# Performance work log

Measured on AMD Instinct MI355X. Metric: run time of the kernel, lower is better.

Reference implementation:

```python
import jax, jax.numpy as jnp
import numpy as np

N_HEADS = 16


def build_bd3lm_mask(n, block_size, dtype):
    """BD3LM mask for concatenated [xt | x0] input of length 2n.
    0 = attend, finfo.min = masked. Shape (2n, 2n)."""
    idx = jnp.arange(2 * n)
    q_idx = idx[:, None]
    kv_idx = idx[None, :]
    x0_q = q_idx >= n
    x0_kv = kv_idx >= n
    block_q = jnp.where(x0_q, (q_idx - n) // block_size, q_idx // block_size)
    block_kv = jnp.where(x0_kv, (kv_idx - n) // block_size, kv_idx // block_size)
    block_diagonal = (block_q == block_kv) & (x0_q == x0_kv)
    offset_block_causal = (block_q > block_kv) & x0_kv & (~x0_q)
    block_causal = (block_q >= block_kv) & x0_kv & x0_q
    can_attend = block_diagonal | offset_block_causal | block_causal
    neg = jnp.finfo(dtype).min
    return jnp.where(can_attend, jnp.array(0, dtype), jnp.array(neg, dtype))


def setup_inputs() -> dict:
    key = jax.random.key(0)
    ks = jax.random.split(key, 5)
    B, T, D = 4, 2048, 1024  # T = 2*L, L = 1024
    s = 1.0 / np.sqrt(D)
    return {
        "x": jax.random.normal(ks[0], (B, T, D), jnp.float32),
        "Wq": jax.random.normal(ks[1], (D, D), jnp.float32) * s,
        "bq": jnp.zeros((D,), jnp.float32),
        "Wk": jax.random.normal(ks[2], (D, D), jnp.float32) * s,
        "bk": jnp.zeros((D,), jnp.float32),
        "Wv": jax.random.normal(ks[3], (D, D), jnp.float32) * s,
        "bv": jnp.zeros((D,), jnp.float32),
        "Wo": jax.random.normal(ks[4], (D, D), jnp.float32) * s,
        "bo": jnp.zeros((D,), jnp.float32),
        "block_size": 4,
    }


def reference(x, Wq, bq, Wk, bk, Wv, bv, Wo, bo, block_size):
    B, T, D = x.shape
    H = N_HEADS
    hd = D // H
    n = T // 2  # length of each copy in [xt | x0]
    mask = build_bd3lm_mask(n, block_size, x.dtype)  # (T, T)

    def split_heads(t):  # (B, T, D) -> (B, H, T, hd)
        return t.reshape(B, T, H, hd).transpose(0, 2, 1, 3)

    q = split_heads(x @ Wq + bq) * (hd ** -0.5)
    k = split_heads(x @ Wk + bk)
    v = split_heads(x @ Wv + bv)
    scores = jnp.einsum("bhqd,bhkd->bhqk", q, k) + mask[None, None]
    attn = jax.nn.softmax(scores, axis=-1)
    ctx = jnp.einsum("bhqk,bhkd->bhqd", attn, v)
    ctx = ctx.transpose(0, 2, 1, 3).reshape(B, T, D)
    return ctx @ Wo + bo
```

## Files before the change

### kernel.cpp

```cpp
#include <hip/hip_runtime.h>
#include <hip/hip_bf16.h>
#include <stdint.h>

typedef __hip_bfloat16 bf16;
typedef short v8s __attribute__((ext_vector_type(8)));
typedef float v4f __attribute__((ext_vector_type(4)));

#define TT   2048
#define DD   1024
#define HH   16
#define HDIM 64
#define NN   1024
#define MASKV (-1e9f)
#define QSCALE 0.18033688011112042f

#if __has_builtin(__builtin_amdgcn_exp2f)
#define EXP2F(x) __builtin_amdgcn_exp2f(x)
#else
#define EXP2F(x) exp2f(x)
#endif

__device__ __forceinline__ v4f mfma16x16x32(v8s a, v8s b, v4f c) {
    return __builtin_amdgcn_mfma_f32_16x16x32_bf16(a, b, c, 0, 0, 0);
}

#define GLDS16(lds, g)                                                          \
    __builtin_amdgcn_global_load_lds(                                           \
        (const __attribute__((address_space(1))) void*)(g),                     \
        (__attribute__((address_space(3))) void*)(lds), 16, 0, 0)

__device__ __forceinline__ bf16 f2b(float f) { return __float2bfloat16(f); }

__global__ __launch_bounds__(256) void cast_x(const float* __restrict__ x,
                                              bf16* __restrict__ xb)
{
    const size_t i = ((size_t)blockIdx.x * 256 + threadIdx.x) * 4;
    const float4 f = *(const float4*)(x + i);
    union { bf16 b[4]; uint64_t u; } cv;
    cv.b[0] = f2b(f.x); cv.b[1] = f2b(f.y); cv.b[2] = f2b(f.z); cv.b[3] = f2b(f.w);
    *(uint64_t*)(xb + i) = cv.u;
}

__global__ __launch_bounds__(256) void transpose_w(
    const float* __restrict__ w0, const float* __restrict__ w1,
    const float* __restrict__ w2, const float* __restrict__ w3,
    bf16* __restrict__ dst)
{
    __shared__ float tile[64][65];
    const float* src = (blockIdx.z == 0) ? w0 : (blockIdx.z == 1) ? w1
                      : (blockIdx.z == 2) ? w2 : w3;
    bf16* d = dst + (size_t)blockIdx.z * 1024 * 1024;
    const int r0 = blockIdx.y * 64, c0 = blockIdx.x * 64;
    const int tx = threadIdx.x, ty = threadIdx.y;
#pragma unroll
    for (int j = 0; j < 16; j++) {
        int r = ty + j * 4;
        tile[r][tx] = src[(size_t)(r0 + r) * 1024 + c0 + tx];
    }
    __syncthreads();
#pragma unroll
    for (int j = 0; j < 16; j++) {
        int r = ty + j * 4;
        d[(size_t)(c0 + r) * 1024 + r0 + tx] = f2b(tile[tx][r]);
    }
}

__global__ __launch_bounds__(256) void transpose_v(
    const bf16* __restrict__ vtmp, bf16* __restrict__ vt)
{
    __shared__ bf16 tile[64][66];
    const int bh = blockIdx.y, t0 = blockIdx.x * 64;
    const int tx = threadIdx.x, ty = threadIdx.y;
    const bf16* src = vtmp + (size_t)bh * TT * HDIM;
    bf16* dst = vt + (size_t)bh * HDIM * TT;
#pragma unroll
    for (int j = 0; j < 16; j++) {
        int r = ty + j * 4;
        tile[r][tx] = src[(size_t)(t0 + r) * HDIM + tx];
    }
    __syncthreads();
#pragma unroll
    for (int j = 0; j < 16; j++) {
        int r = ty + j * 4;
        dst[(size_t)r * TT + t0 + tx] = tile[tx][r];
    }
}

__global__ __launch_bounds__(512, 2) void gemm_qkv(
    const bf16* __restrict__ A, const bf16* __restrict__ BT,
    const float* __restrict__ bq, const float* __restrict__ bk,
    const float* __restrict__ bv,
    bf16* __restrict__ qo, bf16* __restrict__ ko, bf16* __restrict__ vo)
{
    __shared__ __align__(16) bf16 As[2 * 256 * 64];
    __shared__ __align__(16) bf16 Bs[2 * 192 * 64];
    const int K = 1024, NT = K >> 6;

    const int id  = blockIdx.x;
    const int fid = (id & 7) * 64 + (id >> 3);
    const int by  = fid >> 4, bx = fid & 15;
    const int m0  = by * 256, n0 = bx * 192;

    const int tid  = threadIdx.x;
    const int lane = tid & 63, wv = tid >> 6;
    const int quad = lane >> 4, c = lane & 15;
    const int wm = wv >> 2, wn = wv & 3;
    const int c7 = c & 15 & 7;

    const int q8  = lane >> 3;
    const int gsw = ((lane & 7) ^ (q8 & 7)) << 3;
    const bf16* aSrc = A + (size_t)(m0 + wv * 8 + q8) * K + gsw;
    const int vB = wv * 8 + q8;
    const bf16* bSrc = BT + (size_t)(n0 + (vB >> 4) * 48 + (vB & 15)) * K + gsw;

    auto stageA = [&](bf16* dst, int j, int kt) {
        GLDS16(dst + (j * 64 + wv * 8) * 64, aSrc + (size_t)(j * 64) * K + kt * 64);
    };
    auto stageB = [&](bf16* dst, int j, int kt) {
        GLDS16(dst + (j * 64 + wv * 8) * 64, bSrc + (size_t)(j * 16) * K + kt * 64);
    };

    v4f acc[8][3];
#pragma unroll
    for (int i = 0; i < 8; i++)
#pragma unroll
        for (int j = 0; j < 3; j++) acc[i][j] = (v4f){0.f, 0.f, 0.f, 0.f};

    stageB(Bs, 0, 0); stageB(Bs, 1, 0);
    stageA(As, 0, 0); stageA(As, 2, 0);
    stageA(As, 1, 0); stageA(As, 3, 0);
    stageB(Bs, 2, 0);
    asm volatile("s_waitcnt vmcnt(3)" ::: "memory");
    asm volatile("s_barrier" ::: "memory");

    v8s afr[4][2], bfr01[2][2], bfr2[2];
#pragma unroll 1
    for (int kt = 0; kt < NT; ++kt) {
        bf16* Ac = As + (kt & 1) * 16384;
        bf16* Bc = Bs + (kt & 1) * 12288;
        bf16* An = As + ((kt & 1) ^ 1) * 16384;
        bf16* Bn = Bs + ((kt & 1) ^ 1) * 12288;
        const int ktn = (kt + 1 < NT) ? kt + 1 : kt;

#pragma unroll
        for (int nt = 0; nt < 2; nt++)
#pragma unroll
            for (int kh = 0; kh < 2; kh++)
                bfr01[nt][kh] = *(const v8s*)(Bc + (nt * 64 + wn * 16 + c) * 64
                                              + (((kh * 4 + quad) ^ c7) << 3));
#pragma unroll
        for (int mt = 0; mt < 4; mt++)
#pragma unroll
            for (int kh = 0; kh < 2; kh++)
                afr[mt][kh] = *(const v8s*)(Ac + (wm * 128 + mt * 16 + c) * 64
                                            + (((kh * 4 + quad) ^ c7) << 3));
        stageB(Bn, 0, ktn); stageB(Bn, 1, ktn);
        asm volatile("s_barrier" ::: "memory");
        __builtin_amdgcn_s_setprio(1);
#pragma unroll
        for (int mt = 0; mt < 4; mt++)
#pragma unroll
            for (int nt = 0; nt < 2; nt++) {
                acc[mt][nt] = mfma16x16x32(afr[mt][0], bfr01[nt][0], acc[mt][nt]);
                acc[mt][nt] = mfma16x16x32(afr[mt][1], bfr01[nt][1], acc[mt][nt]);
            }
        __builtin_amdgcn_s_setprio(0);
        asm volatile("s_waitcnt vmcnt(3)" ::: "memory");
        asm volatile("s_barrier" ::: "memory");

#pragma unroll
        for (int mt = 0; mt < 4; mt++)
#pragma unroll
            for (int kh = 0; kh < 2; kh++)
                afr[mt][kh] = *(const v8s*)(Ac + (wm * 128 + 64 + mt * 16 + c) * 64
                                            + (((kh * 4 + quad) ^ c7) << 3));
        stageA(An, 0, ktn); stageA(An, 2, ktn);
        asm volatile("s_barrier" ::: "memory");
        __builtin_amdgcn_s_setprio(1);
#pragma unroll
        for (int mt = 0; mt < 4; mt++)
#pragma unroll
            for (int nt = 0; nt < 2; nt++) {
                acc[4 + mt][nt] = mfma16x16x32(afr[mt][0], bfr01[nt][0], acc[4 + mt][nt]);
                acc[4 + mt][nt] = mfma16x16x32(afr[mt][1], bfr01[nt][1], acc[4 + mt][nt]);
            }
        __builtin_amdgcn_s_setprio(0);
        asm volatile("s_waitcnt vmcnt(4)" ::: "memory");
        asm volatile("s_barrier" ::: "memory");

#pragma unroll
        for (int kh = 0; kh < 2; kh++)
            bfr2[kh] = *(const v8s*)(Bc + (128 + wn * 16 + c) * 64
                                     + (((kh * 4 + quad) ^ c7) << 3));
        stageA(An, 1, ktn); stageA(An, 3, ktn);
        asm volatile("s_barrier" ::: "memory");
        __builtin_amdgcn_s_setprio(1);
#pragma unroll
        for (int mt = 0; mt < 4; mt++) {
            acc[4 + mt][2] = mfma16x16x32(afr[mt][0], bfr2[0], acc[4 + mt][2]);
            acc[4 + mt][2] = mfma16x16x32(afr[mt][1], bfr2[1], acc[4 + mt][2]);
        }
        __builtin_amdgcn_s_setprio(0);
        asm volatile("s_barrier" ::: "memory");

#pragma unroll
        for (int mt = 0; mt < 4; mt++)
#pragma unroll
            for (int kh = 0; kh < 2; kh++)
                afr[mt][kh] = *(const v8s*)(Ac + (wm * 128 + mt * 16 + c) * 64
                                            + (((kh * 4 + quad) ^ c7) << 3));
        stageB(Bn, 2, ktn);
        asm volatile("s_barrier" ::: "memory");
        __builtin_amdgcn_s_setprio(1);
#pragma unroll
        for (int mt = 0; mt < 4; mt++) {
            acc[mt][2] = mfma16x16x32(afr[mt][0], bfr2[0], acc[mt][2]);
            acc[mt][2] = mfma16x16x32(afr[mt][1], bfr2[1], acc[mt][2]);
        }
        __builtin_amdgcn_s_setprio(0);
        asm volatile("s_waitcnt vmcnt(3)" ::: "memory");
        asm volatile("s_barrier" ::: "memory");
    }
    asm volatile("s_waitcnt vmcnt(0)" ::: "memory");

#pragma unroll
    for (int i = 0; i < 8; i++)
#pragma unroll
        for (int nt = 0; nt < 3; nt++) {
            const int colb = n0 + wn * 48 + nt * 16;
            const int type = colb >> 10;
            bf16* o = (type == 0) ? qo : (type == 1) ? ko : vo;
            const float* bp = (type == 0) ? bq : (type == 1) ? bk : bv;
            const float scale = (type == 0) ? QSCALE : 1.0f;
            const int within = (colb & 1023) + c;
            const int h = within >> 6, d = within & 63;
            const float bias = bp[within];
#pragma unroll
            for (int r = 0; r < 4; r++) {
                const int row = m0 + wm * 128 + (i >> 2) * 64 + (i & 3) * 16
                                + quad * 4 + r;
                const int b_ = row >> 11, t = row & 2047;
                const int bh = b_ * HH + h;
                o[((size_t)bh * TT + t) * HDIM + d] =
                    f2b((acc[i][nt][r] + bias) * scale);
            }
        }
}

__device__ __forceinline__ void gemm_core_256x128(
    const bf16* __restrict__ A, const bf16* __restrict__ BT,
    const int m0, const int n0, const int K,
    bf16* __restrict__ As, bf16* __restrict__ Bs,
    v4f (&acc)[8][2])
{
    const int tid  = threadIdx.x;
    const int lane = tid & 63, wv = tid >> 6;
    const int quad = lane >> 4, c = lane & 15;
    const int wm = wv >> 2, wn = wv & 3;
    const int c7 = c & 7;
    const int NT = K >> 6;

    const int rloc = wv * 8 + (lane >> 3);
    const int gsw  = ((lane & 7) ^ ((lane >> 3) & 7)) << 3;
    const bf16* aSrc = A  + (size_t)(m0 + rloc) * K + gsw;
    const bf16* bSrc = BT + (size_t)(n0 + rloc) * K + gsw;

#pragma unroll
    for (int i = 0; i < 8; i++)
#pragma unroll
        for (int j = 0; j < 2; j++) acc[i][j] = (v4f){0.f, 0.f, 0.f, 0.f};

    auto stageA = [&](bf16* dst, int j, int kt) {
        const int mo = ((j & 1) << 7) | ((j >> 1) << 6);
        GLDS16(dst + (j * 64 + wv * 8) * 64, aSrc + (size_t)mo * K + kt * 64);
    };
    auto stageB = [&](bf16* dst, int j, int kt) {
        GLDS16(dst + (j * 64 + wv * 8) * 64, bSrc + (size_t)(j << 6) * K + kt * 64);
    };

    stageB(Bs, 0, 0); stageB(Bs, 1, 0);
    stageA(As, 0, 0); stageA(As, 1, 0); stageA(As, 2, 0); stageA(As, 3, 0);
    asm volatile("s_waitcnt vmcnt(2)" ::: "memory");
    asm volatile("s_barrier" ::: "memory");

#pragma unroll 1
    for (int kt = 0; kt < NT; ++kt) {
        bf16* Ac = As + (kt & 1) * 16384;
        bf16* Bc = Bs + (kt & 1) * 8192;
        bf16* An = As + ((kt & 1) ^ 1) * 16384;
        bf16* Bn = Bs + ((kt & 1) ^ 1) * 8192;
        const int ktn = (kt + 1 < NT) ? kt + 1 : kt;

        v8s bfr[2][2];
#pragma unroll
        for (int nt = 0; nt < 2; nt++)
#pragma unroll
            for (int kh = 0; kh < 2; kh++)
                bfr[nt][kh] = *(const v8s*)(Bc + (wn * 32 + nt * 16 + c) * 64
                                            + (((kh * 4 + quad) ^ c7) << 3));
        v8s af[4][2];
#pragma unroll
        for (int mt = 0; mt < 4; mt++)
#pragma unroll
            for (int kh = 0; kh < 2; kh++)
                af[mt][kh] = *(const v8s*)(Ac + (wm * 64 + mt * 16 + c) * 64
                                           + (((kh * 4 + quad) ^ c7) << 3));
        stageB(Bn, 0, ktn); stageB(Bn, 1, ktn); stageA(An, 0, ktn);
        asm volatile("s_barrier" ::: "memory");
        __builtin_amdgcn_s_setprio(1);
#pragma unroll
        for (int mt = 0; mt < 4; mt++)
#pragma unroll
            for (int nt = 0; nt < 2; nt++) {
                acc[mt][nt] = mfma16x16x32(af[mt][0], bfr[nt][0], acc[mt][nt]);
                acc[mt][nt] = mfma16x16x32(af[mt][1], bfr[nt][1], acc[mt][nt]);
            }
        __builtin_amdgcn_s_setprio(0);
        asm volatile("s_waitcnt vmcnt(3)" ::: "memory");
        asm volatile("s_barrier" ::: "memory");

#pragma unroll
        for (int mt = 0; mt < 4; mt++)
#pragma unroll
            for (int kh = 0; kh < 2; kh++)
                af[mt][kh] = *(const v8s*)(Ac + (128 + wm * 64 + mt * 16 + c) * 64
                                           + (((kh * 4 + quad) ^ c7) << 3));
        stageA(An, 1, ktn); stageA(An, 2, ktn); stageA(An, 3, ktn);
        asm volatile("s_barrier" ::: "memory");
        __builtin_amdgcn_s_setprio(1);
#pragma unroll
        for (int mt = 0; mt < 4; mt++)
#pragma unroll
            for (int nt = 0; nt < 2; nt++) {
                acc[4 + mt][nt] = mfma16x16x32(af[mt][0], bfr[nt][0], acc[4 + mt][nt]);
                acc[4 + mt][nt] = mfma16x16x32(af[mt][1], bfr[nt][1], acc[4 + mt][nt]);
            }
        __builtin_amdgcn_s_setprio(0);
        asm volatile("s_waitcnt vmcnt(2)" ::: "memory");
        asm volatile("s_barrier" ::: "memory");
    }
}

__global__ __launch_bounds__(512, 2) void gemm_out(
    const bf16* __restrict__ A, const bf16* __restrict__ BT,
    const float* __restrict__ bo, float* __restrict__ out)
{
    __shared__ __align__(16) bf16 As[2 * 256 * 64];
    __shared__ __align__(16) bf16 Bs[2 * 128 * 64];
    const int id  = blockIdx.x;
    const int fid = (id & 7) * 32 + (id >> 3);
    const int by  = fid >> 3, bx = fid & 7;
    const int m0  = by * 256, n0 = bx * 128;

    v4f acc[8][2];
    gemm_core_256x128(A, BT, m0, n0, 1024, As, Bs, acc);

    const int tid  = threadIdx.x;
    const int lane = tid & 63, wv = tid >> 6;
    const int quad = lane >> 4, c = lane & 15;
    const int wm = wv >> 2, wn = wv & 3;

#pragma unroll
    for (int mt = 0; mt < 8; mt++)
#pragma unroll
        for (int nt = 0; nt < 2; nt++) {
            const int col = n0 + wn * 32 + nt * 16 + c;
            const float bias = bo[col];
#pragma unroll
            for (int r = 0; r < 4; r++) {
                const int row = m0 + wm * 128 + mt * 16 + quad * 4 + r;
                out[(size_t)row * 1024 + col] = acc[mt][nt][r] + bias;
            }
        }
}

__global__ __launch_bounds__(256, 4) void attn(
    const bf16* __restrict__ Q, const bf16* __restrict__ Kb,
    const bf16* __restrict__ VT, bf16* __restrict__ ctx,
    const int* __restrict__ bsp)
{
    __shared__ __align__(16) bf16 Kt[2][32 * 64];
    __shared__ __align__(16) bf16 Vt[2][64 * 32];
    __shared__ __align__(16) bf16 plds[4][2][16 * 32];

    const int bs = bsp[0];
    const float inv  = 1.0f / (float)bs;
    const float hinv = 0.5f * inv;
    const int tid = threadIdx.x, lane = tid & 63, wv = tid >> 6;
    const int quad = lane >> 4, c = lane & 15;
    const int bh = blockIdx.x & 63;
    const int j  = blockIdx.x >> 6;
    const int g_tbl[16] = {7,6,5,4, 0,1,2,3, 4,5,6,7, 3,2,1,0};
    const bool xt = j < 8;
    const int g  = g_tbl[j];
    const int q0g = (xt ? 0 : NN) + g * 128;

    const bf16* qp = Q  + (size_t)bh * TT * HDIM;
    const bf16* kp = Kb + (size_t)bh * TT * HDIM;
    const bf16* vp = VT + (size_t)bh * HDIM * TT;

    int d_lo = 0, nd = 0, nf = 0, b_lo = 0, nb = 0;
    if (xt) {
        d_lo = (bs * (q0g / bs)) & ~31;
        const int d_hi = min((bs * ((q0g + 127) / bs) + bs + 31) & ~31, NN);
        nd = (d_hi - d_lo) >> 5;
        const int f = bs * (q0g / bs);
        nf = f >> 5;
        b_lo = NN + (nf << 5);
        const int b_hi = NN + min((bs * ((q0g + 127) / bs) + 31) & ~31, NN);
        nb = (b_hi > b_lo) ? (b_hi - b_lo) >> 5 : 0;
    } else {
        const int q0l = q0g - NN;
        const int f = min(bs * (q0l / bs) + bs, NN);
        nf = f >> 5;
        b_lo = NN + (nf << 5);
        const int b_hi = NN + min((bs * ((q0l + 127) / bs) + bs + 31) & ~31, NN);
        nb = (b_hi > b_lo) ? (b_hi - b_lo) >> 5 : 0;
    }
    const int nc = nd + nf + nb;

    float bqv[2][4];
#pragma unroll
    for (int t = 0; t < 2; t++)
#pragma unroll
        for (int r = 0; r < 4; r++) {
            const int qrow = q0g + wv * 32 + t * 16 + quad * 4 + r;
            const int qloc = xt ? qrow : qrow - NN;
            bqv[t][r] = floorf(fmaf((float)qloc, inv, hinv));
        }

    v8s aq[2][2];
#pragma unroll
    for (int t = 0; t < 2; t++) {
        const int rowb = q0g + wv * 32 + t * 16;
        aq[t][0] = *(const v8s*)(qp + (size_t)(rowb + c) * HDIM + quad * 8);
        aq[t][1] = *(const v8s*)(qp + (size_t)(rowb + c) * HDIM + 32 + quad * 8);
    }

    v4f O[2][4];
#pragma unroll
    for (int t = 0; t < 2; t++)
#pragma unroll
        for (int dt = 0; dt < 4; dt++) O[t][dt] = (v4f){0.f, 0.f, 0.f, 0.f};
    float lr[2][4] = {{0.f,0.f,0.f,0.f},{0.f,0.f,0.f,0.f}};

    const int klrow = lane >> 3, ks8 = lane & 7;
    const bf16* kSrc0 = kp + (size_t)(wv * 8 + klrow) * HDIM + ((ks8 ^ klrow) << 3);
    const int vlrow = lane >> 2, vs8 = lane & 3;
    const bf16* vSrc0 = vp + (size_t)(wv * 16 + vlrow) * TT + ((vs8 ^ (vlrow & 3)) << 3);

    auto kb_of = [&](int i, int& kb, int& type) {
        if (i < nd)           { kb = d_lo + (i << 5);             type = 1; }
        else if (i < nd + nf) { kb = NN + ((i - nd) << 5);        type = 0; }
        else                  { kb = b_lo + ((i - nd - nf) << 5); type = xt ? 2 : 3; }
    };
    auto stage = [&](int i) {
        int kb, ty; kb_of(i, kb, ty);
        const int sel = i & 1;
        GLDS16(&Kt[sel][wv * 512], kSrc0 + (size_t)kb * HDIM);
        GLDS16(&Vt[sel][wv * 512], vSrc0 + kb);
    };

    stage(0);
    asm volatile("s_waitcnt vmcnt(0)" ::: "memory");
    asm volatile("s_barrier" ::: "memory");

    const int xk = c & 7, xv = c & 3;
    const int pquad = quad << 3;
#pragma unroll 1
    for (int i = 0; i < nc; i++) {
        int kb, type; kb_of(i, kb, type);
        const int sel = i & 1;
        const bf16* Kl = Kt[sel];
        const bf16* Vl = Vt[sel];

        const v8s k0a = *(const v8s*)(Kl + c * 64        + ((quad       ^ xk) << 3));
        const v8s k0b = *(const v8s*)(Kl + c * 64        + (((quad ^ 4) ^ xk) << 3));
        const v8s k1a = *(const v8s*)(Kl + (16 + c) * 64 + ((quad       ^ xk) << 3));
        const v8s k1b = *(const v8s*)(Kl + (16 + c) * 64 + (((quad ^ 4) ^ xk) << 3));
        v8s vf[4];
#pragma unroll
        for (int dt = 0; dt < 4; dt++)
            vf[dt] = *(const v8s*)(Vl + (dt * 16 + c) * 32 + ((quad ^ xv) << 3));

        if (i + 1 < nc) stage(i + 1);

        float bkA = 0.f, bkB = 0.f;
        if (type) {
            const int off = (type == 1) ? 0 : NN;
            bkA = floorf(fmaf((float)(kb + c - off),      inv, hinv));
            bkB = floorf(fmaf((float)(kb + 16 + c - off), inv, hinv));
        }

#pragma unroll
        for (int t = 0; t < 2; t++) {
            v4f Sa = (v4f){0.f, 0.f, 0.f, 0.f};
            v4f Sb = (v4f){0.f, 0.f, 0.f, 0.f};
            Sa = mfma16x16x32(aq[t][0], k0a, Sa);
            Sa = mfma16x16x32(aq[t][1], k0b, Sa);
            Sb = mfma16x16x32(aq[t][0], k1a, Sb);
            Sb = mfma16x16x32(aq[t][1], k1b, Sb);
            bf16* pw = &plds[wv][t][(quad * 4) * 32];
#pragma unroll
            for (int r = 0; r < 4; r++) {
                float sa = Sa[r], sb = Sb[r];
                if (type == 1) {
                    if (bkA != bqv[t][r]) sa = MASKV;
                    if (bkB != bqv[t][r]) sb = MASKV;
                } else if (type == 2) {
                    if (!(bkA < bqv[t][r])) sa = MASKV;
                    if (!(bkB < bqv[t][r])) sb = MASKV;
                } else if (type == 3) {
                    if (!(bkA <= bqv[t][r])) sa = MASKV;
                    if (!(bkB <= bqv[t][r])) sb = MASKV;
                }
                const float pa = EXP2F(sa);
                const float pb = EXP2F(sb);
                lr[t][r] += pa + pb;
                pw[r * 32 + (c ^ pquad)]        = f2b(pa);
                pw[r * 32 + ((c + 16) ^ pquad)] = f2b(pb);
            }
        }
        asm volatile("s_waitcnt lgkmcnt(0)" ::: "memory");
#pragma unroll
        for (int t = 0; t < 2; t++) {
            const v8s pf = *(const v8s*)(&plds[wv][t][c * 32 +
                                        ((quad ^ ((c >> 2) & 3)) << 3)]);
#pragma unroll
            for (int dt = 0; dt < 4; dt++)
                O[t][dt] = mfma16x16x32(pf, vf[dt], O[t][dt]);
        }

        asm volatile("s_waitcnt vmcnt(0)" ::: "memory");
        asm volatile("s_barrier" ::: "memory");
    }

    const int b_ = bh >> 4, h = bh & 15;
#pragma unroll
    for (int t = 0; t < 2; t++)
#pragma unroll
        for (int r = 0; r < 4; r++) {
            float s = lr[t][r];
#pragma unroll
            for (int off = 1; off < 16; off <<= 1) s += __shfl_xor(s, off);
            const float invl = 1.0f / fmaxf(s, 1e-30f);
            const int trow = q0g + wv * 32 + t * 16 + quad * 4 + r;
#pragma unroll
            for (int dt = 0; dt < 4; dt++)
                ctx[((size_t)(b_ * TT + trow)) * DD + h * 64 + dt * 16 + c] =
                    f2b(O[t][dt][r] * invl);
        }
}

extern "C" void kernel_launch(void* const* d_in, const int* in_sizes, int n_in,
                              void* d_out, int out_size, void* d_ws, size_t ws_size,
                              hipStream_t stream)
{
    const float* x  = (const float*)d_in[0];
    const float* Wq = (const float*)d_in[1];
    const float* bq = (const float*)d_in[2];
    const float* Wk = (const float*)d_in[3];
    const float* bk = (const float*)d_in[4];
    const float* Wv = (const float*)d_in[5];
    const float* bv = (const float*)d_in[6];
    const float* Wo = (const float*)d_in[7];
    const float* bo = (const float*)d_in[8];
    const int*  bsp = (const int*)d_in[9];
    float* out = (float*)d_out;

    bf16* ws    = (bf16*)d_ws;
    bf16* xb    = ws;
    bf16* wqkvT = xb + 8388608;
    bf16* woT   = wqkvT + 3 * 1024 * 1024;
    bf16* qbuf  = woT + 1024 * 1024;
    bf16* kbuf  = qbuf + 8388608;
    bf16* vtmp  = kbuf + 8388608;
    bf16* vt    = vtmp + 8388608;
    bf16* ctx   = xb;

    cast_x<<<8192, 256, 0, stream>>>(x, xb);
    transpose_w<<<dim3(16, 16, 4), dim3(64, 4), 0, stream>>>(Wq, Wk, Wv, Wo, wqkvT);
    gemm_qkv<<<512, 512, 0, stream>>>(xb, wqkvT, bq, bk, bv, qbuf, kbuf, vtmp);
    transpose_v<<<dim3(32, 64), dim3(64, 4), 0, stream>>>(vtmp, vt);
    attn<<<1024, 256, 0, stream>>>(qbuf, kbuf, vt, ctx, bsp);
    gemm_out<<<256, 512, 0, stream>>>(ctx, woT, bo, out);
}
```

Baseline: 239.4 us.

## Fuse V transpose into QKV GEMM epilogue and triple-buffer attention K/V

The QKV GEMM epilogue now writes V directly in transposed (bh, d, t) layout with packed 8-byte stores of four consecutive tokens. This removes the separate transpose_v kernel and its extra read and write of V. The attention kernel moves from double to triple buffering of K/V tiles in LDS, prefetching two chunks ahead and waiting with vmcnt(2) instead of vmcnt(0), so load latency overlaps more compute. The costs are more LDS per block, which could lower occupancy, and redundant restaging of the last chunk near the tail.

```diff
diff --git a/kernel.cpp b/kernel.cpp
--- a/kernel.cpp
+++ b/kernel.cpp
@@ -65,32 +65,11 @@
     }
 }
 
-__global__ __launch_bounds__(256) void transpose_v(
-    const bf16* __restrict__ vtmp, bf16* __restrict__ vt)
-{
-    __shared__ bf16 tile[64][66];
-    const int bh = blockIdx.y, t0 = blockIdx.x * 64;
-    const int tx = threadIdx.x, ty = threadIdx.y;
-    const bf16* src = vtmp + (size_t)bh * TT * HDIM;
-    bf16* dst = vt + (size_t)bh * HDIM * TT;
-#pragma unroll
-    for (int j = 0; j < 16; j++) {
-        int r = ty + j * 4;
-        tile[r][tx] = src[(size_t)(t0 + r) * HDIM + tx];
-    }
-    __syncthreads();
-#pragma unroll
-    for (int j = 0; j < 16; j++) {
-        int r = ty + j * 4;
-        dst[(size_t)r * TT + t0 + tx] = tile[tx][r];
-    }
-}
-
 __global__ __launch_bounds__(512, 2) void gemm_qkv(
     const bf16* __restrict__ A, const bf16* __restrict__ BT,
     const float* __restrict__ bq, const float* __restrict__ bk,
     const float* __restrict__ bv,
-    bf16* __restrict__ qo, bf16* __restrict__ ko, bf16* __restrict__ vo)
+    bf16* __restrict__ qo, bf16* __restrict__ ko, bf16* __restrict__ vt)
 {
     __shared__ __align__(16) bf16 As[2 * 256 * 64];
     __shared__ __align__(16) bf16 Bs[2 * 192 * 64];
@@ -105,7 +84,7 @@
     const int lane = tid & 63, wv = tid >> 6;
     const int quad = lane >> 4, c = lane & 15;
     const int wm = wv >> 2, wn = wv & 3;
-    const int c7 = c & 15 & 7;
+    const int c7 = c & 7;
 
     const int q8  = lane >> 3;
     const int gsw = ((lane & 7) ^ (q8 & 7)) << 3;
@@ -221,7 +200,6 @@
         asm volatile("s_waitcnt vmcnt(3)" ::: "memory");
         asm volatile("s_barrier" ::: "memory");
     }
-    asm volatile("s_waitcnt vmcnt(0)" ::: "memory");
 
 #pragma unroll
     for (int i = 0; i < 8; i++)
@@ -229,20 +207,27 @@
         for (int nt = 0; nt < 3; nt++) {
             const int colb = n0 + wn * 48 + nt * 16;
             const int type = colb >> 10;
-            bf16* o = (type == 0) ? qo : (type == 1) ? ko : vo;
-            const float* bp = (type == 0) ? bq : (type == 1) ? bk : bv;
-            const float scale = (type == 0) ? QSCALE : 1.0f;
             const int within = (colb & 1023) + c;
             const int h = within >> 6, d = within & 63;
-            const float bias = bp[within];
-#pragma unroll
-            for (int r = 0; r < 4; r++) {
-                const int row = m0 + wm * 128 + (i >> 2) * 64 + (i & 3) * 16
-                                + quad * 4 + r;
-                const int b_ = row >> 11, t = row & 2047;
-                const int bh = b_ * HH + h;
-                o[((size_t)bh * TT + t) * HDIM + d] =
-                    f2b((acc[i][nt][r] + bias) * scale);
+            const int row0 = m0 + wm * 128 + (i >> 2) * 64 + (i & 3) * 16
+                             + quad * 4;
+            const int b_ = row0 >> 11, t0 = row0 & 2047;
+            const int bh = b_ * HH + h;
+            if (type < 2) {
+                bf16* o = (type == 0) ? qo : ko;
+                const float* bp = (type == 0) ? bq : bk;
+                const float scale = (type == 0) ? QSCALE : 1.0f;
+                const float bias = bp[within];
+#pragma unroll
+                for (int r = 0; r < 4; r++)
+                    o[((size_t)bh * TT + (t0 + r)) * HDIM + d] =
+                        f2b((acc[i][nt][r] + bias) * scale);
+            } else {
+                const float bias = bv[within];
+                union { bf16 b[4]; uint64_t u; } cv;
+#pragma unroll
+                for (int r = 0; r < 4; r++) cv.b[r] = f2b(acc[i][nt][r] + bias);
+                *(uint64_t*)(vt + ((size_t)bh * HDIM + d) * TT + t0) = cv.u;
             }
         }
 }
@@ -379,8 +364,8 @@
     const bf16* __restrict__ VT, bf16* __restrict__ ctx,
     const int* __restrict__ bsp)
 {
-    __shared__ __align__(16) bf16 Kt[2][32 * 64];
-    __shared__ __align__(16) bf16 Vt[2][64 * 32];
+    __shared__ __align__(16) bf16 Kt[3][32 * 64];
+    __shared__ __align__(16) bf16 Vt[3][64 * 32];
     __shared__ __align__(16) bf16 plds[4][2][16 * 32];
 
     const int bs = bsp[0];
@@ -454,23 +439,23 @@
         else if (i < nd + nf) { kb = NN + ((i - nd) << 5);        type = 0; }
         else                  { kb = b_lo + ((i - nd - nf) << 5); type = xt ? 2 : 3; }
     };
-    auto stage = [&](int i) {
-        int kb, ty; kb_of(i, kb, ty);
-        const int sel = i & 1;
-        GLDS16(&Kt[sel][wv * 512], kSrc0 + (size_t)kb * HDIM);
-        GLDS16(&Vt[sel][wv * 512], vSrc0 + kb);
+    auto stage = [&](int ch, int slot) {
+        int kb, ty; kb_of(ch, kb, ty);
+        GLDS16(&Kt[slot][wv * 512], kSrc0 + (size_t)kb * HDIM);
+        GLDS16(&Vt[slot][wv * 512], vSrc0 + kb);
     };
 
-    stage(0);
-    asm volatile("s_waitcnt vmcnt(0)" ::: "memory");
+    stage(0, 0);
+    stage(nc > 1 ? 1 : 0, 1);
+    asm volatile("s_waitcnt vmcnt(2)" ::: "memory");
     asm volatile("s_barrier" ::: "memory");
 
     const int xk = c & 7, xv = c & 3;
     const int pquad = quad << 3;
+    int sel = 0;
 #pragma unroll 1
     for (int i = 0; i < nc; i++) {
         int kb, type; kb_of(i, kb, type);
-        const int sel = i & 1;
         const bf16* Kl = Kt[sel];
         const bf16* Vl = Vt[sel];
 
@@ -483,7 +468,8 @@
         for (int dt = 0; dt < 4; dt++)
             vf[dt] = *(const v8s*)(Vl + (dt * 16 + c) * 32 + ((quad ^ xv) << 3));
 
-        if (i + 1 < nc) stage(i + 1);
+        const int selp2 = (sel >= 1) ? sel - 1 : 2;
+        stage(i + 2 < nc ? i + 2 : nc - 1, selp2);
 
         float bkA = 0.f, bkB = 0.f;
         if (type) {
@@ -531,8 +517,9 @@
                 O[t][dt] = mfma16x16x32(pf, vf[dt], O[t][dt]);
         }
 
-        asm volatile("s_waitcnt vmcnt(0)" ::: "memory");
-        asm volatile("s_barrier" ::: "memory");
+        asm volatile("s_waitcnt vmcnt(2)" ::: "memory");
+        asm volatile("s_barrier" ::: "memory");
+        sel = (sel >= 2) ? 0 : sel + 1;
     }
 
     const int b_ = bh >> 4, h = bh & 15;
@@ -574,14 +561,12 @@
     bf16* woT   = wqkvT + 3 * 1024 * 1024;
     bf16* qbuf  = woT + 1024 * 1024;
     bf16* kbuf  = qbuf + 8388608;
-    bf16* vtmp  = kbuf + 8388608;
-    bf16* vt    = vtmp + 8388608;
+    bf16* vt    = kbuf + 8388608;
     bf16* ctx   = xb;
 
     cast_x<<<8192, 256, 0, stream>>>(x, xb);
     transpose_w<<<dim3(16, 16, 4), dim3(64, 4), 0, stream>>>(Wq, Wk, Wv, Wo, wqkvT);
-    gemm_qkv<<<512, 512, 0, stream>>>(xb, wqkvT, bq, bk, bv, qbuf, kbuf, vtmp);
-    transpose_v<<<dim3(32, 64), dim3(64, 4), 0, stream>>>(vtmp, vt);
+    gemm_qkv<<<512, 512, 0, stream>>>(xb, wqkvT, bq, bk, bv, qbuf, kbuf, vt);
     attn<<<1024, 256, 0, stream>>>(qbuf, kbuf, vt, ctx, bsp);
     gemm_out<<<256, 512, 0, stream>>>(ctx, woT, bo, out);
 }
```

After: 242.1 us. Within noise of the previous version (+1.1%).
